# Optimization experiments

Measured on AMD Instinct MI355X. Metric: run time of the kernel, lower is better.

The kernel has to match this reference:

```python
import jax, jax.numpy as jnp
import numpy as np

NUM_SUPERPIXELS = 256


def setup_inputs() -> dict:
    key = jax.random.key(0)
    k1, k2 = jax.random.split(key)
    B, H, W, C = 8, 512, 512, 64
    feature_map = jax.random.normal(k1, (B, H, W, C), dtype=jnp.float32)
    superpixel_map = jax.random.randint(k2, (B, H, W), 0, NUM_SUPERPIXELS, dtype=jnp.int32)
    return {"feature_map": feature_map, "superpixel_map": superpixel_map}


def reference(feature_map, superpixel_map):
    # feature_map: [B,H,W,C] float; superpixel_map: [B,H,W] int labels in [0, S)
    B, H, W, C = feature_map.shape
    S = NUM_SUPERPIXELS
    num_segments = B * S
    feat = feature_map.reshape(-1, C)                       # [B*H*W, C]
    batch_ids = jnp.arange(B, dtype=jnp.int32)[:, None, None]
    seg = (batch_ids * S + superpixel_map).reshape(-1)      # global segment id [B*H*W]
    sums = jax.ops.segment_sum(feat, seg, num_segments=num_segments)          # [B*S, C]
    counts = jax.ops.segment_sum(jnp.ones((seg.shape[0],), feat.dtype), seg,
                                 num_segments=num_segments)                    # [B*S]
    means = sums / jnp.maximum(counts, 1.0)[:, None]        # empty segments -> 0
    return means.reshape(B, S, C)
```

## Files before the change

kernel.cpp:

```cpp
#include <hip/hip_runtime.h>


#define NBATCH 8
#define NSEG 256
#define NCH 64
#define PPB (512 * 512)
#define GSEG 2
#define NWAVE 8
#define PIX_PER_WAVE (PPB / NWAVE)
#define ITERS (PIX_PER_WAVE / (64 * 4))

__global__ __launch_bounds__(512, 8) void pool_kernel(const float* __restrict__ feat,
                                                      const int* __restrict__ sp,
                                                      float* __restrict__ out) {
    __shared__ float part[NWAVE][GSEG][NCH];
    __shared__ unsigned scnt[NWAVE][GSEG];

    const int b = blockIdx.x >> 7;
    const int sgrp = blockIdx.x & 127;
    const int seg0 = sgrp * 2;
    const int seg1 = seg0 + 1;
    const int lane = threadIdx.x & 63;
    const int wave = threadIdx.x >> 6;

    const int4* lp4 = (const int4*)(sp + (size_t)b * PPB + (size_t)wave * PIX_PER_WAVE);
    const float* fb = feat + (size_t)b * PPB * NCH + lane;

    float acc0 = 0.0f, acc1 = 0.0f;
    unsigned c0 = 0u, c1 = 0u;

    int4 cur = lp4[lane];
    for (int i = 0; i < ITERS; ++i) {
        const int ni = (i + 1 < ITERS) ? (i + 1) : i;
        int4 nxt = lp4[ni * 64 + lane];
        const int base = wave * PIX_PER_WAVE + i * 256;

#define PROC(LV, C)                                                          \
        {                                                                    \
            unsigned long long m0 = __ballot((LV) == seg0);                  \
            unsigned long long m1 = __ballot((LV) == seg1);                  \
            c0 += (unsigned)__builtin_popcountll(m0);                        \
            c1 += (unsigned)__builtin_popcountll(m1);                        \
            while (m0) {                                                     \
                int j = __builtin_ctzll(m0); m0 &= m0 - 1;                   \
                acc0 += fb[(size_t)(base + j * 4 + (C)) * NCH];              \
            }                                                                \
            while (m1) {                                                     \
                int j = __builtin_ctzll(m1); m1 &= m1 - 1;                   \
                acc1 += fb[(size_t)(base + j * 4 + (C)) * NCH];              \
            }                                                                \
        }
        PROC(cur.x, 0)
        PROC(cur.y, 1)
        PROC(cur.z, 2)
        PROC(cur.w, 3)
#undef PROC
        cur = nxt;
    }

    part[wave][0][lane] = acc0;
    part[wave][1][lane] = acc1;
    if (lane == 0) { scnt[wave][0] = c0; scnt[wave][1] = c1; }
    __syncthreads();

    if (threadIdx.x < GSEG * NCH) {
        const int g = threadIdx.x >> 6;
        const int l = threadIdx.x & 63;
        float s = 0.0f;
        unsigned cn = 0u;
#pragma unroll
        for (int w = 0; w < NWAVE; ++w) {
            s += part[w][g][l];
            cn += scnt[w][g];
        }
        const size_t orow = (size_t)b * NSEG + (size_t)(seg0 + g);
        out[orow * NCH + l] = s / (float)(cn > 0u ? cn : 1u);
    }
}

extern "C" void kernel_launch(void* const* d_in, const int* in_sizes, int n_in,
                              void* d_out, int out_size, void* d_ws, size_t ws_size,
                              hipStream_t stream) {
    const float* feat = (const float*)d_in[0];
    const int* sp = (const int*)d_in[1];
    float* out = (float*)d_out;
    (void)d_ws; (void)ws_size;

    pool_kernel<<<NBATCH * (NSEG / GSEG), 512, 0, stream>>>(feat, sp, out);
}
```

Before: 749.6 us.

## Queue matched pixel indices in LDS and gather features in float4 batches

Matched pixel indices are pushed into a per-wave LDS ring buffer instead of being loaded one at a time as 64 scalar floats. Once 16 indices accumulate, the queue is drained with each wave loading 4 pixels at once as float4 per lane, with four independent loads in flight. A cross-slot shuffle reduction runs before the partials are written. The aim is fewer, wider and more overlapped feature loads. The cost is extra LDS traffic and per-match branching, plus possible read-after-write hazards on the queue, since it relies on wave-synchronous execution with no barrier.

```diff
diff --git a/kernel.cpp b/kernel.cpp
--- a/kernel.cpp
+++ b/kernel.cpp
@@ -9,12 +9,15 @@
 #define NWAVE 8
 #define PIX_PER_WAVE (PPB / NWAVE)
 #define ITERS (PIX_PER_WAVE / (64 * 4))
+#define QCAP 32
+#define DRAIN_AT 16
 
 __global__ __launch_bounds__(512, 8) void pool_kernel(const float* __restrict__ feat,
                                                       const int* __restrict__ sp,
                                                       float* __restrict__ out) {
     __shared__ float part[NWAVE][GSEG][NCH];
     __shared__ unsigned scnt[NWAVE][GSEG];
+    __shared__ int q[NWAVE][GSEG][QCAP];
 
     const int b = blockIdx.x >> 7;
     const int sgrp = blockIdx.x & 127;
@@ -22,12 +25,36 @@
     const int seg1 = seg0 + 1;
     const int lane = threadIdx.x & 63;
     const int wave = threadIdx.x >> 6;
+    const int slot = lane >> 4;
+    const int chg  = lane & 15;
 
     const int4* lp4 = (const int4*)(sp + (size_t)b * PPB + (size_t)wave * PIX_PER_WAVE);
-    const float* fb = feat + (size_t)b * PPB * NCH + lane;
+    const float4* fb4 = (const float4*)(feat + (size_t)b * PPB * NCH);
 
-    float acc0 = 0.0f, acc1 = 0.0f;
+    float4 acc0 = {0.f, 0.f, 0.f, 0.f};
+    float4 acc1 = {0.f, 0.f, 0.f, 0.f};
     unsigned c0 = 0u, c1 = 0u;
+    int h0 = 0, t0 = 0, h1 = 0, t1 = 0;
+
+    int* q0 = q[wave][0];
+    int* q1 = q[wave][1];
+
+#define DRAIN16(QP, H, ACC)                                                   \
+    do {                                                                      \
+        int p0_ = QP[(H + 0  + slot) & (QCAP - 1)];                           \
+        int p1_ = QP[(H + 4  + slot) & (QCAP - 1)];                           \
+        int p2_ = QP[(H + 8  + slot) & (QCAP - 1)];                           \
+        int p3_ = QP[(H + 12 + slot) & (QCAP - 1)];                           \
+        float4 v0_ = fb4[(size_t)p0_ * 16 + chg];                             \
+        float4 v1_ = fb4[(size_t)p1_ * 16 + chg];                             \
+        float4 v2_ = fb4[(size_t)p2_ * 16 + chg];                             \
+        float4 v3_ = fb4[(size_t)p3_ * 16 + chg];                             \
+        ACC.x += (v0_.x + v1_.x) + (v2_.x + v3_.x);                           \
+        ACC.y += (v0_.y + v1_.y) + (v2_.y + v3_.y);                           \
+        ACC.z += (v0_.z + v1_.z) + (v2_.z + v3_.z);                           \
+        ACC.w += (v0_.w + v1_.w) + (v2_.w + v3_.w);                           \
+        H += 16;                                                              \
+    } while (0)
 
     int4 cur = lp4[lane];
     for (int i = 0; i < ITERS; ++i) {
@@ -37,17 +64,19 @@
 
 #define PROC(LV, C)                                                          \
         {                                                                    \
-            unsigned long long m0 = __ballot((LV) == seg0);                  \
-            unsigned long long m1 = __ballot((LV) == seg1);                  \
-            c0 += (unsigned)__builtin_popcountll(m0);                        \
-            c1 += (unsigned)__builtin_popcountll(m1);                        \
-            while (m0) {                                                     \
-                int j = __builtin_ctzll(m0); m0 &= m0 - 1;                   \
-                acc0 += fb[(size_t)(base + j * 4 + (C)) * NCH];              \
+            unsigned long long m0_ = __ballot((LV) == seg0);                 \
+            unsigned long long m1_ = __ballot((LV) == seg1);                 \
+            c0 += (unsigned)__builtin_popcountll(m0_);                       \
+            c1 += (unsigned)__builtin_popcountll(m1_);                       \
+            while (m0_) {                                                    \
+                int j = __builtin_ctzll(m0_); m0_ &= m0_ - 1;                \
+                q0[t0 & (QCAP - 1)] = base + j * 4 + (C); t0++;              \
+                if (t0 - h0 >= DRAIN_AT) DRAIN16(q0, h0, acc0);              \
             }                                                                \
-            while (m1) {                                                     \
-                int j = __builtin_ctzll(m1); m1 &= m1 - 1;                   \
-                acc1 += fb[(size_t)(base + j * 4 + (C)) * NCH];              \
+            while (m1_) {                                                    \
+                int j = __builtin_ctzll(m1_); m1_ &= m1_ - 1;                \
+                q1[t1 & (QCAP - 1)] = base + j * 4 + (C); t1++;              \
+                if (t1 - h1 >= DRAIN_AT) DRAIN16(q1, h1, acc1);              \
             }                                                                \
         }
         PROC(cur.x, 0)
@@ -58,8 +87,33 @@
         cur = nxt;
     }
 
-    part[wave][0][lane] = acc0;
-    part[wave][1][lane] = acc1;
+#define TAIL(QP, H, T, ACC)                                                   \
+    while (H < T) {                                                           \
+        int p_ = (H + slot < T) ? QP[(H + slot) & (QCAP - 1)] : -1;           \
+        if (p_ >= 0) {                                                        \
+            float4 v_ = fb4[(size_t)p_ * 16 + chg];                           \
+            ACC.x += v_.x; ACC.y += v_.y; ACC.z += v_.z; ACC.w += v_.w;       \
+        }                                                                     \
+        H += 4;                                                               \
+    }
+    TAIL(q0, h0, t0, acc0)
+    TAIL(q1, h1, t1, acc1)
+#undef TAIL
+#undef DRAIN16
+
+    acc0.x += __shfl_xor(acc0.x, 16); acc0.x += __shfl_xor(acc0.x, 32);
+    acc0.y += __shfl_xor(acc0.y, 16); acc0.y += __shfl_xor(acc0.y, 32);
+    acc0.z += __shfl_xor(acc0.z, 16); acc0.z += __shfl_xor(acc0.z, 32);
+    acc0.w += __shfl_xor(acc0.w, 16); acc0.w += __shfl_xor(acc0.w, 32);
+    acc1.x += __shfl_xor(acc1.x, 16); acc1.x += __shfl_xor(acc1.x, 32);
+    acc1.y += __shfl_xor(acc1.y, 16); acc1.y += __shfl_xor(acc1.y, 32);
+    acc1.z += __shfl_xor(acc1.z, 16); acc1.z += __shfl_xor(acc1.z, 32);
+    acc1.w += __shfl_xor(acc1.w, 16); acc1.w += __shfl_xor(acc1.w, 32);
+
+    if (lane < 16) {
+        ((float4*)part[wave][0])[lane] = acc0;
+        ((float4*)part[wave][1])[lane] = acc1;
+    }
     if (lane == 0) { scnt[wave][0] = c0; scnt[wave][1] = c1; }
     __syncthreads();
 
```

Measured after the change: 707.5 us. -5.6%, faster.

## Replace per-segment ballot scan with shared-memory histogram atomics and global reduction

Applied to the files above, without the earlier changes.

Rather than each block scanning the whole batch's labels for two segments and gathering matching feature values, each block now streams its own slab of pixels once. It reads features as coalesced float4 and accumulates them into a padded shared-memory per-segment histogram with LDS atomics, along with per-segment counts. Block partials are combined with global atomics into the zeroed output, and a separate finalize kernel divides by the counts. This removes the redundant label scans and the uncoalesced scalar gathers. In exchange it adds LDS atomic contention, two memsets, an extra kernel launch, and nondeterministic float summation order.

```diff
diff --git a/kernel.cpp b/kernel.cpp
--- a/kernel.cpp
+++ b/kernel.cpp
@@ -5,77 +5,83 @@
 #define NSEG 256
 #define NCH 64
 #define PPB (512 * 512)
-#define GSEG 2
+#define BLOCKS_PER_BATCH 64
+#define PIX_PER_BLOCK (PPB / BLOCKS_PER_BATCH)
 #define NWAVE 8
-#define PIX_PER_WAVE (PPB / NWAVE)
-#define ITERS (PIX_PER_WAVE / (64 * 4))
+#define PIX_PER_WAVE (PIX_PER_BLOCK / NWAVE)
+#define STAGE_PIX 256
+#define NSTAGE (PIX_PER_WAVE / STAGE_PIX)
+#define STEPS (STAGE_PIX / 4)
+#define HPAD 65
 
-__global__ __launch_bounds__(512, 8) void pool_kernel(const float* __restrict__ feat,
+__global__ __launch_bounds__(512, 4) void pool_kernel(const float* __restrict__ feat,
                                                       const int* __restrict__ sp,
-                                                      float* __restrict__ out) {
-    __shared__ float part[NWAVE][GSEG][NCH];
-    __shared__ unsigned scnt[NWAVE][GSEG];
+                                                      float* __restrict__ outsum,
+                                                      unsigned* __restrict__ cnts) {
+    __shared__ float hist[NSEG][HPAD];
+    __shared__ unsigned cnt[NSEG];
+    __shared__ int lbl[NWAVE][STAGE_PIX];
 
-    const int b = blockIdx.x >> 7;
-    const int sgrp = blockIdx.x & 127;
-    const int seg0 = sgrp * 2;
-    const int seg1 = seg0 + 1;
-    const int lane = threadIdx.x & 63;
-    const int wave = threadIdx.x >> 6;
+    const int b = blockIdx.x >> 6;
+    const int slab = blockIdx.x & 63;
+    const int tid = threadIdx.x;
+    const int lane = tid & 63;
+    const int wave = tid >> 6;
+    const int slot = lane >> 4;
+    const int chg = lane & 15;
 
-    const int4* lp4 = (const int4*)(sp + (size_t)b * PPB + (size_t)wave * PIX_PER_WAVE);
-    const float* fb = feat + (size_t)b * PPB * NCH + lane;
-
-    float acc0 = 0.0f, acc1 = 0.0f;
-    unsigned c0 = 0u, c1 = 0u;
-
-    int4 cur = lp4[lane];
-    for (int i = 0; i < ITERS; ++i) {
-        const int ni = (i + 1 < ITERS) ? (i + 1) : i;
-        int4 nxt = lp4[ni * 64 + lane];
-        const int base = wave * PIX_PER_WAVE + i * 256;
-
-#define PROC(LV, C)                                                          \
-        {                                                                    \
-            unsigned long long m0 = __ballot((LV) == seg0);                  \
-            unsigned long long m1 = __ballot((LV) == seg1);                  \
-            c0 += (unsigned)__builtin_popcountll(m0);                        \
-            c1 += (unsigned)__builtin_popcountll(m1);                        \
-            while (m0) {                                                     \
-                int j = __builtin_ctzll(m0); m0 &= m0 - 1;                   \
-                acc0 += fb[(size_t)(base + j * 4 + (C)) * NCH];              \
-            }                                                                \
-            while (m1) {                                                     \
-                int j = __builtin_ctzll(m1); m1 &= m1 - 1;                   \
-                acc1 += fb[(size_t)(base + j * 4 + (C)) * NCH];              \
-            }                                                                \
-        }
-        PROC(cur.x, 0)
-        PROC(cur.y, 1)
-        PROC(cur.z, 2)
-        PROC(cur.w, 3)
-#undef PROC
-        cur = nxt;
-    }
-
-    part[wave][0][lane] = acc0;
-    part[wave][1][lane] = acc1;
-    if (lane == 0) { scnt[wave][0] = c0; scnt[wave][1] = c1; }
+    for (int i = tid; i < NSEG * HPAD; i += 512) ((float*)hist)[i] = 0.0f;
+    if (tid < NSEG) cnt[tid] = 0u;
     __syncthreads();
 
-    if (threadIdx.x < GSEG * NCH) {
-        const int g = threadIdx.x >> 6;
-        const int l = threadIdx.x & 63;
-        float s = 0.0f;
-        unsigned cn = 0u;
-#pragma unroll
-        for (int w = 0; w < NWAVE; ++w) {
-            s += part[w][g][l];
-            cn += scnt[w][g];
+    const int pix0 = slab * PIX_PER_BLOCK + wave * PIX_PER_WAVE;
+    const int* lp = sp + (size_t)b * PPB + pix0;
+    const float4* fp = (const float4*)(feat + (size_t)b * PPB * NCH) + (size_t)pix0 * 16;
+
+    for (int s = 0; s < NSTAGE; ++s) {
+        int4 lv = ((const int4*)(lp + s * STAGE_PIX))[lane];
+        ((int4*)lbl[wave])[lane] = lv;
+
+        const float4* fs = fp + (size_t)s * STAGE_PIX * 16;
+
+        int l_cur = lbl[wave][slot];
+        float4 v_cur = fs[(size_t)slot * 16 + chg];
+
+        for (int t = 0; t < STEPS; ++t) {
+            const int tn = (t + 1 < STEPS) ? (t + 1) : t;
+            int l_nxt = lbl[wave][4 * tn + slot];
+            float4 v_nxt = fs[(size_t)(4 * tn + slot) * 16 + chg];
+
+            float* hrow = &hist[l_cur][chg * 4];
+            unsafeAtomicAdd(&hrow[0], v_cur.x);
+            unsafeAtomicAdd(&hrow[1], v_cur.y);
+            unsafeAtomicAdd(&hrow[2], v_cur.z);
+            unsafeAtomicAdd(&hrow[3], v_cur.w);
+            if (chg == 0) atomicAdd(&cnt[l_cur], 1u);
+
+            l_cur = l_nxt;
+            v_cur = v_nxt;
         }
-        const size_t orow = (size_t)b * NSEG + (size_t)(seg0 + g);
-        out[orow * NCH + l] = s / (float)(cn > 0u ? cn : 1u);
     }
+    __syncthreads();
+
+    const size_t obase = (size_t)b * NSEG * NCH;
+    for (int i = tid; i < NSEG * NCH; i += 512) {
+        const int seg = i >> 6;
+        const int ch = i & 63;
+        unsafeAtomicAdd(&outsum[obase + i], hist[seg][ch]);
+    }
+    if (tid < NSEG) atomicAdd(&cnts[(size_t)b * NSEG + tid], cnt[tid]);
+}
+
+__global__ void finalize_kernel(float* __restrict__ outsum,
+                                const unsigned* __restrict__ cnts) {
+    const int idx4 = blockIdx.x * blockDim.x + threadIdx.x;
+    const unsigned c = cnts[idx4 >> 4];
+    const float inv = 1.0f / (float)(c > 0u ? c : 1u);
+    float4 v = ((float4*)outsum)[idx4];
+    v.x *= inv; v.y *= inv; v.z *= inv; v.w *= inv;
+    ((float4*)outsum)[idx4] = v;
 }
 
 extern "C" void kernel_launch(void* const* d_in, const int* in_sizes, int n_in,
@@ -84,7 +90,11 @@
     const float* feat = (const float*)d_in[0];
     const int* sp = (const int*)d_in[1];
     float* out = (float*)d_out;
-    (void)d_ws; (void)ws_size;
+    unsigned* cnts = (unsigned*)d_ws;
+    (void)in_sizes; (void)n_in; (void)out_size; (void)ws_size;
 
-    pool_kernel<<<NBATCH * (NSEG / GSEG), 512, 0, stream>>>(feat, sp, out);
+    hipMemsetAsync(d_out, 0, (size_t)NBATCH * NSEG * NCH * sizeof(float), stream);
+    hipMemsetAsync(d_ws, 0, (size_t)NBATCH * NSEG * sizeof(unsigned), stream);
+    pool_kernel<<<NBATCH * BLOCKS_PER_BATCH, 512, 0, stream>>>(feat, sp, out, cnts);
+    finalize_kernel<<<(NBATCH * NSEG * NCH / 4) / 256, 256, 0, stream>>>(out, cnts);
 }
```

Result: slower. 1.207 ms (+61.0%).
